# Kernel optimization log

Hardware: AMD Instinct MI355X
Metric: run time of the kernel (lower is better)

Reference implementation:

```python
import jax, jax.numpy as jnp
import numpy as np

N_NODES = 50000
N_EDGES = 800000
N_GRAPHS = 256
IN_CH = 128
HID = 128
OUT_CH = 10
BN_EPS = 1e-5


def setup_inputs() -> dict:
    key = jax.random.key(0)
    ks = jax.random.split(key, 32)
    x = jax.random.normal(ks[0], (N_NODES, IN_CH), dtype=jnp.float32)
    edge_index = jax.random.randint(ks[1], (2, N_EDGES), 0, N_NODES)
    batch = jnp.sort(jax.random.randint(ks[2], (N_NODES,), 0, N_GRAPHS))

    def lin(k, fan_in, fan_out):
        return (jax.random.normal(k, (fan_in, fan_out), dtype=jnp.float32)
                * np.float32(1.0 / np.sqrt(fan_in)))

    inp = {"x": x, "edge_index": edge_index, "batch": batch}
    dims = [(IN_CH, HID), (HID, HID), (HID, HID)]
    for i, (fi, fo) in enumerate(dims):
        inp[f"W{i}"] = lin(ks[3 + i], fi, fo)
        inp[f"b{i}"] = jnp.zeros((fo,), jnp.float32)
        inp[f"g{i}"] = jnp.ones((fo,), jnp.float32)
        inp[f"be{i}"] = jnp.zeros((fo,), jnp.float32)
    inp["lin1_w"] = lin(ks[10], 2 * HID, HID)
    inp["lin1_b"] = jnp.zeros((HID,), jnp.float32)
    inp["lin2_w"] = lin(ks[11], HID, OUT_CH)
    inp["lin2_b"] = jnp.zeros((OUT_CH,), jnp.float32)
    return inp


def _gcn_conv(x, W, b, src, dst):
    # PyG GCNConv: h = X W; add self-loops; symmetric D^-1/2 (A+I) D^-1/2 aggregation.
    h = x @ W  # [N, F]
    loops = jnp.arange(N_NODES)
    s = jnp.concatenate([src, loops])
    d = jnp.concatenate([dst, loops])
    deg = jax.ops.segment_sum(jnp.ones_like(d, jnp.float32), d, num_segments=N_NODES)
    dinv = jnp.where(deg > 0, jax.lax.rsqrt(deg), 0.0)
    coef = dinv[s] * dinv[d]  # [E+N]
    out = jax.ops.segment_sum(h[s] * coef[:, None], d, num_segments=N_NODES)
    return out + b


def _batch_norm(x, gamma, beta):
    mean = x.mean(axis=0)
    var = x.var(axis=0)
    return (x - mean) * jax.lax.rsqrt(var + BN_EPS) * gamma + beta


def _forward(x, edge_index, batch,
             W0, b0, g0, be0, W1, b1, g1, be1, W2, b2, g2, be2,
             lin1_w, lin1_b, lin2_w, lin2_b):
    src, dst = edge_index[0], edge_index[1]
    for W, b, g, be in ((W0, b0, g0, be0), (W1, b1, g1, be1), (W2, b2, g2, be2)):
        x = _gcn_conv(x, W, b, src, dst)
        x = jax.nn.relu(_batch_norm(x, g, be))
    x_sum = jax.ops.segment_sum(x, batch, num_segments=N_GRAPHS)  # [G, H]
    counts = jax.ops.segment_sum(jnp.ones((N_NODES,), jnp.float32), batch,
                                 num_segments=N_GRAPHS)
    x_mean = x_sum / jnp.maximum(counts, 1.0)[:, None]
    h = jnp.concatenate([x_mean, x_sum], axis=1)  # [G, 2H]
    h = jax.nn.relu(h @ lin1_w + lin1_b)
    return h @ lin2_w + lin2_b  # [G, OUT_CH]


def reference(x, edge_index, batch,
              W0, b0, g0, be0, W1, b1, g1, be1, W2, b2, g2, be2,
              lin1_w, lin1_b, lin2_w, lin2_b):
    return _forward(x, edge_index, batch,
                    W0, b0, g0, be0, W1, b1, g1, be1, W2, b2, g2, be2,
                    lin1_w, lin1_b, lin2_w, lin2_b)
```

## Files before the change

kernel.cpp:

```cpp
#include <hip/hip_runtime.h>

#define N_NODES 50000
#define N_EDGES 800000
#define N_GRAPHS 256
#define HID 128
#define OUT_CH 10
#define BN_EPS 1e-5f

#define NBUCKET 98
#define BCAP 10240
#define BN_BLOCKS 1024

#define OFF_H       0
#define OFF_BNPART  2937856
#define OFF_CSRD    3200000
#define OFF_WBT     4000000
#define OFF_AGG     6400000
#define OFF_ROWPTR  12850000
#define OFF_CSR     12950004
#define OFF_DINV    13750004
#define OFF_BNCOEF  13800004
#define OFF_BCNT    13833284

#define WBT_PITCH 136

typedef __attribute__((ext_vector_type(8))) short bf16x8;
typedef __attribute__((ext_vector_type(4))) float f32x4;

__device__ __forceinline__ ushort f2bf(float f) {
    union { float f; unsigned u; } v; v.f = f;
    unsigned r = v.u + 0x7FFFu + ((v.u >> 16) & 1u);
    return (ushort)(r >> 16);
}
__device__ __forceinline__ float bf2f(unsigned u16) {
    return __uint_as_float(u16 << 16);
}

__global__ void k_zero(int* bcnt) {
    int i = threadIdx.x;
    if (i < NBUCKET) bcnt[i] = 0;
}

__global__ __launch_bounds__(256) void k_bucket(const int* __restrict__ ei,
                                                int* __restrict__ bcnt,
                                                int2* __restrict__ buf) {
    __shared__ int histL[NBUCKET], baseL[NBUCKET], curL[NBUCKET];
    int t = threadIdx.x;
    if (t < NBUCKET) histL[t] = 0;
    __syncthreads();
    const int stride = gridDim.x * 256;
    for (int i = blockIdx.x * 256 + t; i < N_EDGES; i += stride)
        atomicAdd(&histL[ei[N_EDGES + i] >> 9], 1);
    __syncthreads();
    if (t < NBUCKET) {
        baseL[t] = atomicAdd(&bcnt[t], histL[t]);
        curL[t] = 0;
    }
    __syncthreads();
    for (int i = blockIdx.x * 256 + t; i < N_EDGES; i += stride) {
        int s = ei[i];
        int d = ei[N_EDGES + i];
        int b = d >> 9;
        int p = baseL[b] + atomicAdd(&curL[b], 1);
        if (p < BCAP) buf[b * BCAP + p] = make_int2(s, d);
    }
}

__global__ __launch_bounds__(512) void k_csrbuild(const int2* __restrict__ buf,
                                                  const int* __restrict__ bcnt,
                                                  int* __restrict__ rowptr,
                                                  int* __restrict__ csr,
                                                  float* __restrict__ dinv) {
    __shared__ int off[512];
    __shared__ int cur[512];
    __shared__ int ebase_s;
    int b = blockIdx.x, t = threadIdx.x;
    int node0 = b << 9;
    int cnt = bcnt[b];
    const int2* mybuf = buf + b * BCAP;

    if (t == 0) {
        int acc = 0;
        for (int i = 0; i < b; ++i) acc += bcnt[i];
        ebase_s = acc;
        if (b == NBUCKET - 1) rowptr[N_NODES] = acc + cnt;
    }
    off[t] = 0;
    __syncthreads();
    int ebase = ebase_s;
    for (int e = t; e < cnt; e += 512)
        atomicAdd(&off[mybuf[e].y - node0], 1);
    __syncthreads();
    int mydeg = off[t];
    for (int o = 1; o < 512; o <<= 1) {
        int x = (t >= o) ? off[t - o] : 0;
        __syncthreads();
        off[t] += x;
        __syncthreads();
    }
    int inc = off[t];
    cur[t] = ebase + inc - mydeg;
    int node = node0 + t;
    if (node < N_NODES) {
        rowptr[node] = ebase + inc - mydeg;
        dinv[node] = rsqrtf((float)(mydeg + 1));
    }
    __syncthreads();
    for (int e = t; e < cnt; e += 512) {
        int2 pr = mybuf[e];
        int p = atomicAdd(&cur[pr.y - node0], 1);
        csr[p] = pr.x;
    }
}

__global__ __launch_bounds__(256) void k_sortseg(const int* __restrict__ rowptr,
                                                 int* __restrict__ csr,
                                                 const float* __restrict__ dinv,
                                                 float* __restrict__ csrd) {
    int wave = threadIdx.x >> 6, lane = threadIdx.x & 63;
    int v = blockIdx.x * 4 + wave;
    if (v >= N_NODES) return;
    int e0 = rowptr[v], deg = rowptr[v + 1] - e0;
    if (deg <= 64) {
        int val = (lane < deg) ? csr[e0 + lane] : 0x7FFFFFFF;
#pragma unroll
        for (int k = 2; k <= 64; k <<= 1)
#pragma unroll
            for (int j = k >> 1; j > 0; j >>= 1) {
                int other = __shfl_xor(val, j);
                bool up = ((lane & k) == 0);
                bool lower = ((lane & j) == 0);
                int mn = min(val, other), mx = max(val, other);
                val = (up == lower) ? mn : mx;
            }
        if (lane < deg) {
            csr[e0 + lane] = val;
            csrd[e0 + lane] = dinv[val];
        }
    } else {
        if (lane == 0) {
            for (int i = e0 + 1; i < e0 + deg; ++i) {
                int key = csr[i];
                int j = i - 1;
                while (j >= e0 && csr[j] > key) { csr[j + 1] = csr[j]; --j; }
                csr[j + 1] = key;
            }
        }
        for (int e = e0 + lane; e < e0 + deg; e += 64) csrd[e] = dinv[csr[e]];
    }
}

__global__ void k_wprep3(const float* __restrict__ W0, const float* __restrict__ W1,
                         const float* __restrict__ W2, ushort* __restrict__ Wbt) {
    int i = blockIdx.x * 256 + threadIdx.x;
    if (i < 3 * 16384) {
        int layer = i / 16384, r = i - layer * 16384;
        const float* W = (layer == 0) ? W0 : (layer == 1) ? W1 : W2;
        int k = r >> 7, c = r & 127;
        Wbt[layer * 128 * WBT_PITCH + c * WBT_PITCH + k] = f2bf(W[r]);
    }
}

template <int BN>
__global__ __launch_bounds__(256) void k_gemm(const float* __restrict__ X,
                                              const ushort* __restrict__ Wbt,
                                              ushort* __restrict__ Hb,
                                              const float* __restrict__ coef,
                                              int nrows) {
    __shared__ __align__(16) ushort Wt[128 * WBT_PITCH];
    int t = threadIdx.x;
    for (int i = t; i < 2176; i += 256)
        ((uint4*)Wt)[i] = ((const uint4*)Wbt)[i];
    __syncthreads();

    int wv = t >> 6, l = t & 63;
    int m = l & 15;
    int kg = l >> 4;
    int row = blockIdx.x * 64 + wv * 16 + m;
    bool valid = row < nrows;
    const float* xr = X + (long)row * 128;

    f32x4 acc[8];
#pragma unroll
    for (int n = 0; n < 8; ++n) acc[n] = (f32x4){0.f, 0.f, 0.f, 0.f};

#pragma unroll
    for (int t4 = 0; t4 < 4; ++t4) {
        int k0 = t4 * 32 + kg * 8;
        float xv[8];
        if (valid) {
            float4 u0 = *(const float4*)(xr + k0);
            float4 u1 = *(const float4*)(xr + k0 + 4);
            if (BN) {
                float4 s0 = *(const float4*)(coef + k0);
                float4 s1 = *(const float4*)(coef + k0 + 4);
                float4 h0 = *(const float4*)(coef + 128 + k0);
                float4 h1 = *(const float4*)(coef + 128 + k0 + 4);
                u0.x = fmaxf(u0.x * s0.x + h0.x, 0.f);
                u0.y = fmaxf(u0.y * s0.y + h0.y, 0.f);
                u0.z = fmaxf(u0.z * s0.z + h0.z, 0.f);
                u0.w = fmaxf(u0.w * s0.w + h0.w, 0.f);
                u1.x = fmaxf(u1.x * s1.x + h1.x, 0.f);
                u1.y = fmaxf(u1.y * s1.y + h1.y, 0.f);
                u1.z = fmaxf(u1.z * s1.z + h1.z, 0.f);
                u1.w = fmaxf(u1.w * s1.w + h1.w, 0.f);
            }
            xv[0] = u0.x; xv[1] = u0.y; xv[2] = u0.z; xv[3] = u0.w;
            xv[4] = u1.x; xv[5] = u1.y; xv[6] = u1.z; xv[7] = u1.w;
        } else {
#pragma unroll
            for (int j = 0; j < 8; ++j) xv[j] = 0.f;
        }
        union { ushort u[8]; bf16x8 v; } A;
#pragma unroll
        for (int j = 0; j < 8; ++j) A.u[j] = f2bf(xv[j]);

#pragma unroll
        for (int n = 0; n < 8; ++n) {
            bf16x8 b = *(const bf16x8*)(&Wt[(n * 16 + m) * WBT_PITCH + k0]);
            acc[n] = __builtin_amdgcn_mfma_f32_16x16x32_bf16(A.v, b, acc[n], 0, 0, 0);
        }
    }

    int srow0 = blockIdx.x * 64 + wv * 16 + kg * 4;
#pragma unroll
    for (int n = 0; n < 8; ++n)
#pragma unroll
        for (int r = 0; r < 4; ++r) {
            int rr = srow0 + r;
            if (rr < nrows) Hb[(long)rr * 128 + n * 16 + m] = f2bf(acc[n][r]);
        }
}

__global__ __launch_bounds__(256) void k_agg(const ushort* __restrict__ Hb,
                                             const int* __restrict__ rowptr,
                                             const int* __restrict__ csr,
                                             const float* __restrict__ csrd,
                                             const float* __restrict__ dinv,
                                             const float* __restrict__ bias,
                                             float* __restrict__ OUT) {
    int wave = threadIdx.x >> 6, lane = threadIdx.x & 63;
    int v = blockIdx.x * 4 + wave;
    if (v >= N_NODES) return;
    int q = lane >> 4, ql = lane & 15;
    int c = ql * 8;
    float dv = dinv[v];
    int e0 = rowptr[v];
    int deg = rowptr[v + 1] - e0;
    float a0 = 0.f, a1 = 0.f, a2 = 0.f, a3 = 0.f;
    float a4 = 0.f, a5 = 0.f, a6 = 0.f, a7 = 0.f;

    for (int base = 0; base < deg; base += 64) {
        int mye = base + lane;
        int idx = 0; float dvi = 0.f;
        if (mye < deg) { idx = csr[e0 + mye]; dvi = csrd[e0 + mye]; }
        int n = min(64, deg - base);
        int P = (n + 3) >> 2;
        int p = 0;
#define EDGE(pp) { \
        int sl = 4 * (pp) + q; \
        int s = __shfl(idx, sl); \
        float cf = __shfl(dvi, sl) * dv; \
        uint4 qv = *(const uint4*)(Hb + (long)s * 128 + c); \
        a0 += cf * bf2f(qv.x & 0xFFFFu); \
        a1 += cf * bf2f(qv.x >> 16); \
        a2 += cf * bf2f(qv.y & 0xFFFFu); \
        a3 += cf * bf2f(qv.y >> 16); \
        a4 += cf * bf2f(qv.z & 0xFFFFu); \
        a5 += cf * bf2f(qv.z >> 16); \
        a6 += cf * bf2f(qv.w & 0xFFFFu); \
        a7 += cf * bf2f(qv.w >> 16); }
        for (; p + 4 <= P; p += 4) { EDGE(p) EDGE(p + 1) EDGE(p + 2) EDGE(p + 3) }
        for (; p < P; ++p) { EDGE(p) }
#undef EDGE
    }
    a0 += __shfl_xor(a0, 16); a0 += __shfl_xor(a0, 32);
    a1 += __shfl_xor(a1, 16); a1 += __shfl_xor(a1, 32);
    a2 += __shfl_xor(a2, 16); a2 += __shfl_xor(a2, 32);
    a3 += __shfl_xor(a3, 16); a3 += __shfl_xor(a3, 32);
    a4 += __shfl_xor(a4, 16); a4 += __shfl_xor(a4, 32);
    a5 += __shfl_xor(a5, 16); a5 += __shfl_xor(a5, 32);
    a6 += __shfl_xor(a6, 16); a6 += __shfl_xor(a6, 32);
    a7 += __shfl_xor(a7, 16); a7 += __shfl_xor(a7, 32);
    if (q == 0) {
        uint4 qv = *(const uint4*)(Hb + (long)v * 128 + c);
        float cs = dv * dv;
        float4 b0 = *(const float4*)(bias + c);
        float4 b1 = *(const float4*)(bias + c + 4);
        float4 o0, o1;
        o0.x = a0 + cs * bf2f(qv.x & 0xFFFFu) + b0.x;
        o0.y = a1 + cs * bf2f(qv.x >> 16) + b0.y;
        o0.z = a2 + cs * bf2f(qv.y & 0xFFFFu) + b0.z;
        o0.w = a3 + cs * bf2f(qv.y >> 16) + b0.w;
        o1.x = a4 + cs * bf2f(qv.z & 0xFFFFu) + b1.x;
        o1.y = a5 + cs * bf2f(qv.z >> 16) + b1.y;
        o1.z = a6 + cs * bf2f(qv.w & 0xFFFFu) + b1.z;
        o1.w = a7 + cs * bf2f(qv.w >> 16) + b1.w;
        *(float4*)(OUT + (long)v * 128 + c) = o0;
        *(float4*)(OUT + (long)v * 128 + c + 4) = o1;
    }
}

__global__ __launch_bounds__(256) void k_bnstats(const float* __restrict__ X,
                                                 float* __restrict__ part) {
    int ch = threadIdx.x & 127;
    int half = threadIdx.x >> 7;
    float s = 0.f, q = 0.f;
    for (int v = blockIdx.x * 2 + half; v < N_NODES; v += BN_BLOCKS * 2) {
        float x = X[(long)v * 128 + ch];
        s += x;
        q += x * x;
    }
    __shared__ float sh[256];
    sh[threadIdx.x] = s;
    __syncthreads();
    float s2 = (half == 0) ? s + sh[threadIdx.x + 128] : 0.f;
    __syncthreads();
    sh[threadIdx.x] = q;
    __syncthreads();
    if (half == 0) {
        float q2 = q + sh[threadIdx.x + 128];
        part[blockIdx.x * 256 + ch] = s2;
        part[blockIdx.x * 256 + 128 + ch] = q2;
    }
}

__global__ void k_bnred(const float* __restrict__ part, const float* __restrict__ g,
                        const float* __restrict__ be, float* __restrict__ coef) {
    int t = threadIdx.x;
    int ch = t & 127, stat = t >> 7;
    float acc = 0.f;
    for (int b = 0; b < BN_BLOCKS; ++b) acc += part[b * 256 + stat * 128 + ch];
    __shared__ float sh[256];
    sh[t] = acc;
    __syncthreads();
    if (stat == 0) {
        float inv_n = 1.0f / (float)N_NODES;
        float mean = acc * inv_n;
        float var = sh[128 + ch] * inv_n - mean * mean;
        float sc = g[ch] * rsqrtf(var + BN_EPS);
        coef[ch] = sc;
        coef[128 + ch] = be[ch] - mean * sc;
    }
}

__global__ __launch_bounds__(1024) void k_poolmlp(const float* __restrict__ X,
                                                  const int* __restrict__ batch,
                                                  const float* __restrict__ coef,
                                                  const float* __restrict__ w1,
                                                  const float* __restrict__ b1,
                                                  const float* __restrict__ w2,
                                                  const float* __restrict__ b2,
                                                  float* __restrict__ out) {
    __shared__ int bounds[2];
    __shared__ float red[32][128];
    __shared__ float h[256];
    __shared__ float h1[128];
    int g = blockIdx.x, t = threadIdx.x;
    if (t < 2) {
        int target = g + t;
        int lo = 0, hi = N_NODES;
        while (lo < hi) {
            int mid = (lo + hi) >> 1;
            if (batch[mid] < target) lo = mid + 1; else hi = mid;
        }
        bounds[t] = lo;
    }
    __syncthreads();
    int start = bounds[0], end = bounds[1];
    int way = t >> 5;
    int cg = (t & 31) << 2;
    float4 sc = *(const float4*)(coef + cg);
    float4 sh = *(const float4*)(coef + 128 + cg);
    float4 acc = make_float4(0.f, 0.f, 0.f, 0.f);
    for (int v = start + way; v < end; v += 32) {
        float4 xv = *(const float4*)(X + (long)v * 128 + cg);
        acc.x += fmaxf(xv.x * sc.x + sh.x, 0.f);
        acc.y += fmaxf(xv.y * sc.y + sh.y, 0.f);
        acc.z += fmaxf(xv.z * sc.z + sh.z, 0.f);
        acc.w += fmaxf(xv.w * sc.w + sh.w, 0.f);
    }
    *(float4*)(&red[way][cg]) = acc;
    __syncthreads();
#pragma unroll
    for (int off = 16; off > 0; off >>= 1) {
        if (way < off) {
            float4 a = *(float4*)(&red[way][cg]);
            float4 b = *(float4*)(&red[way + off][cg]);
            a.x += b.x; a.y += b.y; a.z += b.z; a.w += b.w;
            *(float4*)(&red[way][cg]) = a;
        }
        __syncthreads();
    }
    if (way == 0) {
        float4 s = *(float4*)(&red[0][cg]);
        float inv = 1.0f / fmaxf((float)(end - start), 1.0f);
        h[cg] = s.x * inv; h[cg + 1] = s.y * inv;
        h[cg + 2] = s.z * inv; h[cg + 3] = s.w * inv;
        h[128 + cg] = s.x; h[128 + cg + 1] = s.y;
        h[128 + cg + 2] = s.z; h[128 + cg + 3] = s.w;
    }
    __syncthreads();
    int o1 = t & 127, w8 = t >> 7;
    float a = 0.f;
    int i0 = w8 * 32;
#pragma unroll 8
    for (int i = i0; i < i0 + 32; ++i) a += h[i] * w1[i * 128 + o1];
    red[w8][o1] = a;
    __syncthreads();
    if (w8 == 0) {
        float s = b1[o1];
#pragma unroll
        for (int k = 0; k < 8; ++k) s += red[k][o1];
        h1[o1] = fmaxf(s, 0.f);
    }
    __syncthreads();
    if (t < OUT_CH) {
        float o = b2[t];
#pragma unroll 4
        for (int j = 0; j < 128; ++j) o += h1[j] * w2[j * OUT_CH + t];
        out[g * OUT_CH + t] = o;
    }
}

extern "C" void kernel_launch(void* const* d_in, const int* in_sizes, int n_in,
                              void* d_out, int out_size, void* d_ws, size_t ws_size,
                              hipStream_t stream) {
    const float* x = (const float*)d_in[0];
    const int* ei = (const int*)d_in[1];
    const int* batch = (const int*)d_in[2];
    const float* W[3] = {(const float*)d_in[3], (const float*)d_in[7], (const float*)d_in[11]};
    const float* b[3] = {(const float*)d_in[4], (const float*)d_in[8], (const float*)d_in[12]};
    const float* gm[3] = {(const float*)d_in[5], (const float*)d_in[9], (const float*)d_in[13]};
    const float* be[3] = {(const float*)d_in[6], (const float*)d_in[10], (const float*)d_in[14]};
    const float* w1 = (const float*)d_in[15];
    const float* b1 = (const float*)d_in[16];
    const float* w2 = (const float*)d_in[17];
    const float* b2 = (const float*)d_in[18];
    float* out = (float*)d_out;

    float* ws = (float*)d_ws;
    ushort* Hb = (ushort*)(ws + OFF_H);
    float* bnpart = ws + OFF_BNPART;
    float* csrd = ws + OFF_CSRD;
    ushort* Wbt = (ushort*)(ws + OFF_WBT);
    float* AGG = ws + OFF_AGG;
    int2* bucketBuf = (int2*)(ws + OFF_AGG);
    int* rowptr = (int*)(ws + OFF_ROWPTR);
    int* csr = (int*)(ws + OFF_CSR);
    float* dinv = ws + OFF_DINV;
    float* bncoef = ws + OFF_BNCOEF;
    int* bcnt = (int*)(ws + OFF_BCNT);

    const int nb_node4 = (N_NODES + 3) / 4;

    hipLaunchKernelGGL(k_zero, dim3(1), dim3(128), 0, stream, bcnt);
    hipLaunchKernelGGL(k_bucket, dim3(392), dim3(256), 0, stream, ei, bcnt, bucketBuf);
    hipLaunchKernelGGL(k_csrbuild, dim3(NBUCKET), dim3(512), 0, stream,
                       bucketBuf, bcnt, rowptr, csr, dinv);
    hipLaunchKernelGGL(k_sortseg, dim3(nb_node4), dim3(256), 0, stream,
                       rowptr, csr, dinv, csrd);
    hipLaunchKernelGGL(k_wprep3, dim3(192), dim3(256), 0, stream,
                       W[0], W[1], W[2], Wbt);

    const int gemm_blocks = (N_NODES + 63) / 64;
    for (int layer = 0; layer < 3; ++layer) {
        const float* cur_x = (layer == 0) ? x : AGG;
        const ushort* wbt_l = Wbt + layer * 128 * WBT_PITCH;
        if (layer == 0) {
            hipLaunchKernelGGL(k_gemm<0>, dim3(gemm_blocks), dim3(256), 0, stream,
                               cur_x, wbt_l, Hb, (const float*)nullptr, N_NODES);
        } else {
            hipLaunchKernelGGL(k_gemm<1>, dim3(gemm_blocks), dim3(256), 0, stream,
                               cur_x, wbt_l, Hb, bncoef, N_NODES);
        }
        hipLaunchKernelGGL(k_agg, dim3(nb_node4), dim3(256), 0, stream,
                           Hb, rowptr, csr, csrd, dinv, b[layer], AGG);
        hipLaunchKernelGGL(k_bnstats, dim3(BN_BLOCKS), dim3(256), 0, stream, AGG, bnpart);
        hipLaunchKernelGGL(k_bnred, dim3(1), dim3(256), 0, stream,
                           bnpart, gm[layer], be[layer], bncoef);
    }

    hipLaunchKernelGGL(k_poolmlp, dim3(N_GRAPHS), dim3(1024), 0, stream,
                       AGG, batch, bncoef, w1, b1, w2, b2, out);
}
```

Before: 407.8 us.

## Merge zero and weight-prep kernels, widen bnred, hoist self-load, double bucket grid

Folds the bucket-counter zeroing into the weight-conversion kernel, which removes one launch. The single-block BN reduction now uses 1024 threads, each quarter summing a slice of the partials, so the serial loop per thread is shorter. The aggregation kernel issues the self-node feature load before the edge loop so its latency overlaps the neighbour gathers. The bucket kernel grid is doubled to spread the histogram pass across more blocks. Together these are meant to trim launch overhead and serial tails, at the cost of slightly more register pressure in the aggregation kernel and more global atomics on the bucket counters.

```diff
diff --git a/kernel.cpp b/kernel.cpp
--- a/kernel.cpp
+++ b/kernel.cpp
@@ -36,9 +36,17 @@
     return __uint_as_float(u16 << 16);
 }
 
-__global__ void k_zero(int* bcnt) {
-    int i = threadIdx.x;
-    if (i < NBUCKET) bcnt[i] = 0;
+__global__ void k_prep(const float* __restrict__ W0, const float* __restrict__ W1,
+                       const float* __restrict__ W2, ushort* __restrict__ Wbt,
+                       int* __restrict__ bcnt) {
+    int i = blockIdx.x * 256 + threadIdx.x;
+    if (blockIdx.x == 0 && threadIdx.x < NBUCKET) bcnt[threadIdx.x] = 0;
+    if (i < 3 * 16384) {
+        int layer = i / 16384, r = i - layer * 16384;
+        const float* W = (layer == 0) ? W0 : (layer == 1) ? W1 : W2;
+        int k = r >> 7, c = r & 127;
+        Wbt[layer * 128 * WBT_PITCH + c * WBT_PITCH + k] = f2bf(W[r]);
+    }
 }
 
 __global__ __launch_bounds__(256) void k_bucket(const int* __restrict__ ei,
@@ -147,17 +155,6 @@
             }
         }
         for (int e = e0 + lane; e < e0 + deg; e += 64) csrd[e] = dinv[csr[e]];
-    }
-}
-
-__global__ void k_wprep3(const float* __restrict__ W0, const float* __restrict__ W1,
-                         const float* __restrict__ W2, ushort* __restrict__ Wbt) {
-    int i = blockIdx.x * 256 + threadIdx.x;
-    if (i < 3 * 16384) {
-        int layer = i / 16384, r = i - layer * 16384;
-        const float* W = (layer == 0) ? W0 : (layer == 1) ? W1 : W2;
-        int k = r >> 7, c = r & 127;
-        Wbt[layer * 128 * WBT_PITCH + c * WBT_PITCH + k] = f2bf(W[r]);
     }
 }
 
@@ -247,6 +244,8 @@
     float dv = dinv[v];
     int e0 = rowptr[v];
     int deg = rowptr[v + 1] - e0;
+    uint4 qv_self = make_uint4(0u, 0u, 0u, 0u);
+    if (q == 0) qv_self = *(const uint4*)(Hb + (long)v * 128 + c);
     float a0 = 0.f, a1 = 0.f, a2 = 0.f, a3 = 0.f;
     float a4 = 0.f, a5 = 0.f, a6 = 0.f, a7 = 0.f;
 
@@ -283,19 +282,18 @@
     a6 += __shfl_xor(a6, 16); a6 += __shfl_xor(a6, 32);
     a7 += __shfl_xor(a7, 16); a7 += __shfl_xor(a7, 32);
     if (q == 0) {
-        uint4 qv = *(const uint4*)(Hb + (long)v * 128 + c);
         float cs = dv * dv;
         float4 b0 = *(const float4*)(bias + c);
         float4 b1 = *(const float4*)(bias + c + 4);
         float4 o0, o1;
-        o0.x = a0 + cs * bf2f(qv.x & 0xFFFFu) + b0.x;
-        o0.y = a1 + cs * bf2f(qv.x >> 16) + b0.y;
-        o0.z = a2 + cs * bf2f(qv.y & 0xFFFFu) + b0.z;
-        o0.w = a3 + cs * bf2f(qv.y >> 16) + b0.w;
-        o1.x = a4 + cs * bf2f(qv.z & 0xFFFFu) + b1.x;
-        o1.y = a5 + cs * bf2f(qv.z >> 16) + b1.y;
-        o1.z = a6 + cs * bf2f(qv.w & 0xFFFFu) + b1.z;
-        o1.w = a7 + cs * bf2f(qv.w >> 16) + b1.w;
+        o0.x = a0 + cs * bf2f(qv_self.x & 0xFFFFu) + b0.x;
+        o0.y = a1 + cs * bf2f(qv_self.x >> 16) + b0.y;
+        o0.z = a2 + cs * bf2f(qv_self.y & 0xFFFFu) + b0.z;
+        o0.w = a3 + cs * bf2f(qv_self.y >> 16) + b0.w;
+        o1.x = a4 + cs * bf2f(qv_self.z & 0xFFFFu) + b1.x;
+        o1.y = a5 + cs * bf2f(qv_self.z >> 16) + b1.y;
+        o1.z = a6 + cs * bf2f(qv_self.w & 0xFFFFu) + b1.z;
+        o1.w = a7 + cs * bf2f(qv_self.w >> 16) + b1.w;
         *(float4*)(OUT + (long)v * 128 + c) = o0;
         *(float4*)(OUT + (long)v * 128 + c + 4) = o1;
     }
@@ -325,19 +323,29 @@
     }
 }
 
-__global__ void k_bnred(const float* __restrict__ part, const float* __restrict__ g,
-                        const float* __restrict__ be, float* __restrict__ coef) {
+__global__ __launch_bounds__(1024) void k_bnred(const float* __restrict__ part,
+                                                const float* __restrict__ g,
+                                                const float* __restrict__ be,
+                                                float* __restrict__ coef) {
+    __shared__ float sh[4][256];
     int t = threadIdx.x;
-    int ch = t & 127, stat = t >> 7;
+    int st = t & 255;
+    int quarter = t >> 8;
     float acc = 0.f;
-    for (int b = 0; b < BN_BLOCKS; ++b) acc += part[b * 256 + stat * 128 + ch];
-    __shared__ float sh[256];
-    sh[t] = acc;
-    __syncthreads();
-    if (stat == 0) {
+    int b0 = quarter * (BN_BLOCKS / 4);
+    for (int b = b0; b < b0 + BN_BLOCKS / 4; ++b) acc += part[b * 256 + st];
+    sh[quarter][st] = acc;
+    __syncthreads();
+    if (quarter == 0) {
+        float total = ((sh[0][st] + sh[1][st]) + sh[2][st]) + sh[3][st];
+        sh[0][st] = total;
+    }
+    __syncthreads();
+    if (t < 128) {
+        int ch = t;
         float inv_n = 1.0f / (float)N_NODES;
-        float mean = acc * inv_n;
-        float var = sh[128 + ch] * inv_n - mean * mean;
+        float mean = sh[0][ch] * inv_n;
+        float var = sh[0][128 + ch] * inv_n - mean * mean;
         float sc = g[ch] * rsqrtf(var + BN_EPS);
         coef[ch] = sc;
         coef[128 + ch] = be[ch] - mean * sc;
@@ -454,14 +462,13 @@
 
     const int nb_node4 = (N_NODES + 3) / 4;
 
-    hipLaunchKernelGGL(k_zero, dim3(1), dim3(128), 0, stream, bcnt);
-    hipLaunchKernelGGL(k_bucket, dim3(392), dim3(256), 0, stream, ei, bcnt, bucketBuf);
+    hipLaunchKernelGGL(k_prep, dim3(192), dim3(256), 0, stream,
+                       W[0], W[1], W[2], Wbt, bcnt);
+    hipLaunchKernelGGL(k_bucket, dim3(784), dim3(256), 0, stream, ei, bcnt, bucketBuf);
     hipLaunchKernelGGL(k_csrbuild, dim3(NBUCKET), dim3(512), 0, stream,
                        bucketBuf, bcnt, rowptr, csr, dinv);
     hipLaunchKernelGGL(k_sortseg, dim3(nb_node4), dim3(256), 0, stream,
                        rowptr, csr, dinv, csrd);
-    hipLaunchKernelGGL(k_wprep3, dim3(192), dim3(256), 0, stream,
-                       W[0], W[1], W[2], Wbt);
 
     const int gemm_blocks = (N_NODES + 63) / 64;
     for (int layer = 0; layer < 3; ++layer) {
@@ -477,7 +484,7 @@
         hipLaunchKernelGGL(k_agg, dim3(nb_node4), dim3(256), 0, stream,
                            Hb, rowptr, csr, csrd, dinv, b[layer], AGG);
         hipLaunchKernelGGL(k_bnstats, dim3(BN_BLOCKS), dim3(256), 0, stream, AGG, bnpart);
-        hipLaunchKernelGGL(k_bnred, dim3(1), dim3(256), 0, stream,
+        hipLaunchKernelGGL(k_bnred, dim3(1), dim3(1024), 0, stream,
                            bnpart, gm[layer], be[layer], bncoef);
     }
 
```

Result: slower. 558.9 us (+37.0%).
